# Kernel optimization log

Hardware: AMD Instinct MI355X
Metric: run time of the kernel (lower is better)

Reference implementation:

```python
import jax, jax.numpy as jnp
import numpy as np

BATCH = 128
IN_CH, OUT_CH = 64, 64
IN_DIM, OUT_DIM = 4096, 4096
IN_HALF = IN_DIM // 2 + 1    # 2049
OUT_HALF = OUT_DIM // 2 + 1  # 2049
MODES = max(IN_HALF, OUT_HALF)


def setup_inputs() -> dict:
    key = jax.random.key(0)
    k1, k2, k3 = jax.random.split(key, 3)
    scale = 1.0 / np.sqrt(IN_CH * OUT_CH)
    x = jax.random.normal(k1, (BATCH, IN_CH, IN_DIM), dtype=jnp.float32)
    # torch.rand(..., dtype=cfloat) draws U[0,1) for real and imag parts independently
    w_real = jax.random.uniform(k2, (IN_CH, OUT_CH, MODES), dtype=jnp.float32) * scale
    w_imag = jax.random.uniform(k3, (IN_CH, OUT_CH, MODES), dtype=jnp.float32) * scale
    b_real = jnp.zeros((OUT_CH, MODES), dtype=jnp.float32)
    b_imag = jnp.zeros((OUT_CH, MODES), dtype=jnp.float32)
    return {"x": x, "w_real": w_real, "w_imag": w_imag, "b_real": b_real, "b_imag": b_imag}


def _fftfreq_k(n):
    # torch.fft.fftfreq(n) * n -> integer wavenumbers [0,1,...,-1]
    return (jnp.fft.fftfreq(n) * n).astype(jnp.float32)


def reference(x, w_real, w_imag, b_real, b_imag):
    k_in = _fftfreq_k(IN_HALF)    # [IN_HALF]
    k_out = _fftfreq_k(OUT_HALF)  # [OUT_HALF]

    # --- shift_phase ---
    z = jnp.fft.rfft(x)                    # [B, Cin, IN_HALF] complex64
    phi = jnp.angle(z[..., 1])             # [B, Cin] phase of first nonzero mode
    z = z * jnp.exp(-1j * (phi[..., None] * k_in))  # align phases
    phi0 = phi[..., 0:1]                   # [B, 1]

    # pad mode axis up to MODES (no-op when IN_HALF == MODES)
    z = jnp.pad(z, ((0, 0), (0, 0), (0, MODES - IN_HALF)))

    # complex per-mode channel mixing + bias
    w = w_real + 1j * w_imag               # [Cin, Cout, MODES]
    b = b_real + 1j * b_imag               # [Cout, MODES]
    out_ft = jnp.einsum('bix,iox->box', z, w) + b
    out_ft = out_ft[..., :OUT_HALF]        # [B, Cout, OUT_HALF]

    # --- unshift_phase ---
    out_ft = out_ft * jnp.exp(1j * (phi0[..., None] * k_out))  # broadcast [B,1,OUT_HALF]
    return jnp.fft.irfft(out_ft, n=OUT_DIM)  # [B, Cout, OUT_DIM]
```

## Files before the change

kernel.cpp:

```cpp
#include <hip/hip_runtime.h>
#include <math.h>

#define NFFT 4096
#define MH   2048
#define HALF 2049
#define NSIG 8192
#define KT   32
#define NKT  65
#define PAD(e) ((e) + ((e) >> 3))

__device__ __forceinline__ float2 cmulf(float2 a, float2 b) {
  return make_float2(a.x*b.x - a.y*b.y, a.x*b.y + a.y*b.x);
}
__device__ __forceinline__ float2 f2add(float2 a, float2 b){ return make_float2(a.x+b.x, a.y+b.y); }
__device__ __forceinline__ float2 f2sub(float2 a, float2 b){ return make_float2(a.x-b.x, a.y-b.y); }
template<int S> __device__ __forceinline__ float2 mulJ(float2 v){
  return (S < 0) ? make_float2(v.y, -v.x) : make_float2(-v.y, v.x);
}
template<int S> __device__ __forceinline__ void dft4(const float2 a[4], float2 X[4]){
  float2 t0 = f2add(a[0],a[2]), t1 = f2sub(a[0],a[2]);
  float2 t2 = f2add(a[1],a[3]), t3 = f2sub(a[1],a[3]);
  X[0] = f2add(t0,t2); X[2] = f2sub(t0,t2);
  float2 j3 = mulJ<S>(t3);
  X[1] = f2add(t1,j3); X[3] = f2sub(t1,j3);
}
template<int S> __device__ __forceinline__ void dft8(const float2 x[8], float2 X[8]){
  float2 e[4] = {x[0],x[2],x[4],x[6]}, o[4] = {x[1],x[3],x[5],x[7]};
  float2 E[4], O[4]; dft4<S>(e,E); dft4<S>(o,O);
  const float c = 0.70710678118654752f;
  float2 o1 = cmulf(O[1], make_float2(c, (float)S*c));
  float2 o2 = mulJ<S>(O[2]);
  float2 o3 = cmulf(O[3], make_float2(-c, (float)S*c));
  X[0]=f2add(E[0],O[0]); X[4]=f2sub(E[0],O[0]);
  X[1]=f2add(E[1],o1);   X[5]=f2sub(E[1],o1);
  X[2]=f2add(E[2],o2);   X[6]=f2sub(E[2],o2);
  X[3]=f2add(E[3],o3);   X[7]=f2sub(E[3],o3);
}

template<int S>
__device__ __forceinline__ void fft2048(float2* buf, const int tid) {
  #pragma unroll
  for (int lg = 0; lg < 3; ++lg) {
    const int s  = 1 << (3*lg);
    const int q  = tid & (s - 1);
    const int ps = tid - q;
    float2 x[8];
    #pragma unroll
    for (int m = 0; m < 8; ++m) x[m] = buf[PAD(tid + (m << 8))];
    float2 X[8]; dft8<S>(x, X);
    const float th = (float)S * (6.283185307179586f / 2048.0f) * (float)ps;
    float sn, cs; __sincosf(th, &sn, &cs);
    const float2 w1 = make_float2(cs, sn);
    float2 wm = w1;
    X[1] = cmulf(X[1], w1);
    #pragma unroll
    for (int m = 2; m < 8; ++m) { wm = cmulf(wm, w1); X[m] = cmulf(X[m], wm); }
    __syncthreads();
    const int base = q + (ps << 3);
    #pragma unroll
    for (int t = 0; t < 8; ++t) buf[PAD(base + s*t)] = X[t];
    __syncthreads();
  }
  {
    float2 a0[4], a1[4], X0[4], X1[4];
    #pragma unroll
    for (int m = 0; m < 4; ++m) { a0[m] = buf[PAD(tid + (m<<9))]; a1[m] = buf[PAD(tid + 256 + (m<<9))]; }
    dft4<S>(a0, X0); dft4<S>(a1, X1);
    #pragma unroll
    for (int t = 0; t < 4; ++t) { buf[PAD(tid + (t<<9))] = X0[t]; buf[PAD(tid + 256 + (t<<9))] = X1[t]; }
    __syncthreads();
  }
}

__global__ __launch_bounds__(256) void k_rfft_phase(
    const float* __restrict__ x, float2* __restrict__ z, float* __restrict__ phi0) {
  __shared__ float2 buf[2304];
  const int bi  = blockIdx.x;
  const int tid = threadIdx.x;
  const float2* xp = (const float2*)(x + (size_t)bi * NFFT);
  for (int j = tid; j < MH; j += 256) buf[PAD(j)] = xp[j];
  __syncthreads();
  fft2048<-1>(buf, tid);

  {
    const float2 Y1 = buf[PAD(1)], Ym = buf[PAD(2047)];
    const float2 E = make_float2(0.5f*(Y1.x + Ym.x), 0.5f*(Y1.y - Ym.y));
    const float2 D = make_float2(0.5f*(Y1.x - Ym.x), 0.5f*(Y1.y + Ym.y));
    float sn, cs; __sincosf(6.283185307179586f / 4096.0f, &sn, &cs);
    const float2 Z1 = make_float2(E.x + (-sn*D.x + cs*D.y), E.y + (-sn*D.y - cs*D.x));
    const float phi = atan2f(Z1.y, Z1.x);
    if (tid == 0 && (bi & 63) == 0) phi0[bi >> 6] = phi;
    for (int k = tid; k < HALF; k += 256) {
      float2 Zk;
      if (k < MH) {
        const float2 Yk = buf[PAD(k)];
        const float2 Ymk = buf[PAD((MH - k) & (MH - 1))];
        const float2 Ek = make_float2(0.5f*(Yk.x + Ymk.x), 0.5f*(Yk.y - Ymk.y));
        const float2 Dk = make_float2(0.5f*(Yk.x - Ymk.x), 0.5f*(Yk.y + Ymk.y));
        float snk, csk; __sincosf(6.283185307179586f * (float)k / 4096.0f, &snk, &csk);
        Zk = make_float2(Ek.x + (-snk*Dk.x + csk*Dk.y), Ek.y + (-snk*Dk.y - csk*Dk.x));
      } else {
        const float2 Y0 = buf[PAD(0)];
        Zk = make_float2(Y0.x - Y0.y, 0.0f);
      }
      const int kin = (k <= 1024) ? k : k - HALF;
      double rev = (double)phi * (double)kin * 0.15915494309189535;
      rev -= rint(rev);
      const float thr = (float)(rev * 6.283185307179586);
      float snr, csr; __sincosf(thr, &snr, &csr);
      const float2 r = make_float2(Zk.x*csr + Zk.y*snr, Zk.y*csr - Zk.x*snr);
      z[((size_t)(k >> 5) * NSIG + bi) * KT + (k & 31)] = r;
    }
  }
}

__global__ __launch_bounds__(256) void k_gemm_mode(
    float2* __restrict__ zio,
    const float* __restrict__ wr, const float* __restrict__ wi,
    const float* __restrict__ br, const float* __restrict__ bim,
    const float* __restrict__ phi0) {
  __shared__ float4 zst[2][4][128];
  const int t  = threadIdx.x;
  const int kk = t & 31;
  const int g  = t >> 5;
  const int o0 = g * 8;
  const int kt = blockIdx.y;
  const int b0 = blockIdx.x * 4;
  const int k  = kt * KT + kk;
  const bool kvalid = (k < HALF);
  const int kc = kvalid ? k : (HALF - 1);

  const int sb = t >> 6;
  const int sh = t & 63;

  float2 acc[4][8];
  #pragma unroll
  for (int bb = 0; bb < 4; ++bb)
    #pragma unroll
    for (int oo = 0; oo < 8; ++oo) acc[bb][oo] = make_float2(0.f, 0.f);

  const size_t tilebase = (size_t)kt * NSIG * KT;

  {
    const float4* s4 = (const float4*)(zio + tilebase + (size_t)((b0 + sb) * 64) * KT);
    zst[0][sb][sh]      = s4[sh];
    zst[0][sb][sh + 64] = s4[sh + 64];
  }

  #pragma unroll 1
  for (int c = 0; c < 8; ++c) {
    float4 p0, p1;
    if (c < 7) {
      const float4* s4 = (const float4*)(zio + tilebase + (size_t)((b0 + sb) * 64 + (c + 1) * 8) * KT);
      p0 = s4[sh]; p1 = s4[sh + 64];
    }
    __syncthreads();
    #pragma unroll 2
    for (int il = 0; il < 8; ++il) {
      const int i = c * 8 + il;
      float2 zv[4];
      #pragma unroll
      for (int bb = 0; bb < 4; ++bb)
        zv[bb] = ((const float2*)&zst[c & 1][bb][0])[il * KT + kk];
      const float* wrp = wr + ((size_t)i * 64 + o0) * HALF + kc;
      const float* wip = wi + ((size_t)i * 64 + o0) * HALF + kc;
      float wvr[8], wvi[8];
      #pragma unroll
      for (int oo = 0; oo < 8; ++oo) { wvr[oo] = wrp[(size_t)oo * HALF]; wvi[oo] = wip[(size_t)oo * HALF]; }
      #pragma unroll
      for (int oo = 0; oo < 8; ++oo)
        #pragma unroll
        for (int bb = 0; bb < 4; ++bb) {
          acc[bb][oo].x += zv[bb].x * wvr[oo] - zv[bb].y * wvi[oo];
          acc[bb][oo].y += zv[bb].x * wvi[oo] + zv[bb].y * wvr[oo];
        }
    }
    if (c < 7) {
      zst[(c + 1) & 1][sb][sh]      = p0;
      zst[(c + 1) & 1][sb][sh + 64] = p1;
    }
  }
  __syncthreads();

  const int kout = (k <= 1024) ? k : k - HALF;
  #pragma unroll
  for (int bb = 0; bb < 4; ++bb) {
    double rev = (double)phi0[b0 + bb] * (double)kout * 0.15915494309189535;
    rev -= rint(rev);
    const float th = (float)(rev * 6.283185307179586);
    float sn, cs; __sincosf(th, &sn, &cs);
    const float2 rot = make_float2(cs, sn);
    #pragma unroll
    for (int oo = 0; oo < 8; ++oo) {
      const int o = o0 + oo;
      const float2 v = make_float2(acc[bb][oo].x + br[(size_t)o * HALF + kc],
                                   acc[bb][oo].y + bim[(size_t)o * HALF + kc]);
      if (kvalid)
        zio[tilebase + (size_t)((b0 + bb) * 64 + o) * KT + kk] = cmulf(v, rot);
    }
  }
}

__global__ __launch_bounds__(256) void k_irfft(
    const float2* __restrict__ oft, float* __restrict__ out) {
  __shared__ float2 buf[2304];
  const int bo  = blockIdx.x;
  const int tid = threadIdx.x;

  for (int k = tid; k <= 1024; k += 256) {
    const float2 Zk_raw = oft[((size_t)(k >> 5) * NSIG + bo) * KT + (k & 31)];
    if (k == 0) {
      const float2 Zn_raw = oft[((size_t)(MH >> 5) * NSIG + bo) * KT + 0];
      const float2 Zk = make_float2(Zk_raw.x, 0.f);
      const float2 Zm = make_float2(Zn_raw.x, 0.f);
      buf[PAD(0)] = make_float2(0.5f * (Zk.x + Zm.x), 0.5f * (Zk.x - Zm.x));
    } else {
      const int m = MH - k;
      const float2 Zm_raw = (k == 1024) ? Zk_raw
          : oft[((size_t)(m >> 5) * NSIG + bo) * KT + (m & 31)];
      {
        const float2 A = make_float2(Zk_raw.x + Zm_raw.x, Zk_raw.y - Zm_raw.y);
        const float2 D = make_float2(Zk_raw.x - Zm_raw.x, Zk_raw.y + Zm_raw.y);
        float sn, cs; __sincosf(6.283185307179586f * (float)k / 4096.0f, &sn, &cs);
        buf[PAD(k)] = make_float2(0.5f*(A.x + (-sn*D.x - cs*D.y)),
                                  0.5f*(A.y + (-sn*D.y + cs*D.x)));
      }
      if (k != 1024) {
        const float2 A = make_float2(Zm_raw.x + Zk_raw.x, Zm_raw.y - Zk_raw.y);
        const float2 D = make_float2(Zm_raw.x - Zk_raw.x, Zm_raw.y + Zk_raw.y);
        float sn, cs; __sincosf(6.283185307179586f * (float)m / 4096.0f, &sn, &cs);
        buf[PAD(m)] = make_float2(0.5f*(A.x + (-sn*D.x - cs*D.y)),
                                  0.5f*(A.y + (-sn*D.y + cs*D.x)));
      }
    }
  }
  __syncthreads();
  fft2048<1>(buf, tid);

  const float s = 1.0f / (float)MH;
  float2* op = (float2*)(out + (size_t)bo * NFFT);
  for (int n = tid; n < MH; n += 256) {
    const float2 y = buf[PAD(n)];
    op[n] = make_float2(y.x * s, y.y * s);
  }
}

extern "C" void kernel_launch(void* const* d_in, const int* in_sizes, int n_in,
                              void* d_out, int out_size, void* d_ws, size_t ws_size,
                              hipStream_t stream) {
  const float* x   = (const float*)d_in[0];
  const float* wr  = (const float*)d_in[1];
  const float* wi  = (const float*)d_in[2];
  const float* br  = (const float*)d_in[3];
  const float* bim = (const float*)d_in[4];
  float* out = (float*)d_out;

  char* ws = (char*)d_ws;
  float*  phi0 = (float*)ws;
  float2* zA   = (float2*)(ws + 4096);

  k_rfft_phase<<<NSIG, 256, 0, stream>>>(x, zA, phi0);
  k_gemm_mode<<<dim3(32, NKT), 256, 0, stream>>>(zA, wr, wi, br, bim, phi0);
  k_irfft<<<NSIG, 256, 0, stream>>>(zA, out);
}
```

Measured before the change: 630.2 us.

## Pack spectral weights into bf16 pairs in a transposed layout for mode GEMM

Result: slower. 1.005 ms (+59.4%).

```diff
diff --git a/kernel.cpp b/kernel.cpp
--- a/kernel.cpp
+++ b/kernel.cpp
@@ -70,6 +70,25 @@
     for (int t = 0; t < 4; ++t) { buf[PAD(tid + (t<<9))] = X0[t]; buf[PAD(tid + 256 + (t<<9))] = X1[t]; }
     __syncthreads();
   }
+}
+
+__device__ __forceinline__ unsigned short f2bf(float f){
+  unsigned int u = __float_as_uint(f);
+  u = (u + 0x7fffu + ((u >> 16) & 1u)) >> 16;
+  return (unsigned short)u;
+}
+
+__global__ __launch_bounds__(256) void k_wtrans(
+    const float* __restrict__ wr, const float* __restrict__ wi, unsigned int* __restrict__ wt) {
+  const int blk = blockIdx.x;
+  const int og = blk & 7, i = (blk >> 3) & 63, kt = blk >> 9;
+  const int t = threadIdx.x, kk = t & 31, oo = t >> 5;
+  const int o = og * 8 + oo;
+  const int k = kt * KT + kk;
+  const int kc = (k < HALF) ? k : (HALF - 1);
+  const size_t src = (size_t)(i * 64 + o) * HALF + kc;
+  const unsigned int u = (unsigned int)f2bf(wr[src]) | ((unsigned int)f2bf(wi[src]) << 16);
+  wt[(((size_t)kt * 64 + i) * 64 + o) * KT + kk] = u;
 }
 
 __global__ __launch_bounds__(256) void k_rfft_phase(
@@ -115,8 +134,7 @@
 }
 
 __global__ __launch_bounds__(256) void k_gemm_mode(
-    float2* __restrict__ zio,
-    const float* __restrict__ wr, const float* __restrict__ wi,
+    float2* __restrict__ zio, const unsigned int* __restrict__ wt,
     const float* __restrict__ br, const float* __restrict__ bim,
     const float* __restrict__ phi0) {
   __shared__ float4 zst[2][4][128];
@@ -140,6 +158,7 @@
     for (int oo = 0; oo < 8; ++oo) acc[bb][oo] = make_float2(0.f, 0.f);
 
   const size_t tilebase = (size_t)kt * NSIG * KT;
+  const unsigned int* wbase = wt + (((size_t)kt * 64) * 64 + o0) * KT + kk;
 
   {
     const float4* s4 = (const float4*)(zio + tilebase + (size_t)((b0 + sb) * 64) * KT);
@@ -162,18 +181,18 @@
       #pragma unroll
       for (int bb = 0; bb < 4; ++bb)
         zv[bb] = ((const float2*)&zst[c & 1][bb][0])[il * KT + kk];
-      const float* wrp = wr + ((size_t)i * 64 + o0) * HALF + kc;
-      const float* wip = wi + ((size_t)i * 64 + o0) * HALF + kc;
-      float wvr[8], wvi[8];
+      const unsigned int* wp = wbase + (size_t)i * 64 * KT;
       #pragma unroll
-      for (int oo = 0; oo < 8; ++oo) { wvr[oo] = wrp[(size_t)oo * HALF]; wvi[oo] = wip[(size_t)oo * HALF]; }
-      #pragma unroll
-      for (int oo = 0; oo < 8; ++oo)
+      for (int oo = 0; oo < 8; ++oo) {
+        const unsigned int wv = wp[oo * KT];
+        const float wrv = __uint_as_float(wv << 16);
+        const float wiv = __uint_as_float(wv & 0xffff0000u);
         #pragma unroll
         for (int bb = 0; bb < 4; ++bb) {
-          acc[bb][oo].x += zv[bb].x * wvr[oo] - zv[bb].y * wvi[oo];
-          acc[bb][oo].y += zv[bb].x * wvi[oo] + zv[bb].y * wvr[oo];
+          acc[bb][oo].x += zv[bb].x * wrv - zv[bb].y * wiv;
+          acc[bb][oo].y += zv[bb].x * wiv + zv[bb].y * wrv;
         }
+      }
     }
     if (c < 7) {
       zst[(c + 1) & 1][sb][sh]      = p0;
@@ -211,9 +230,7 @@
     const float2 Zk_raw = oft[((size_t)(k >> 5) * NSIG + bo) * KT + (k & 31)];
     if (k == 0) {
       const float2 Zn_raw = oft[((size_t)(MH >> 5) * NSIG + bo) * KT + 0];
-      const float2 Zk = make_float2(Zk_raw.x, 0.f);
-      const float2 Zm = make_float2(Zn_raw.x, 0.f);
-      buf[PAD(0)] = make_float2(0.5f * (Zk.x + Zm.x), 0.5f * (Zk.x - Zm.x));
+      buf[PAD(0)] = make_float2(0.5f * (Zk_raw.x + Zn_raw.x), 0.5f * (Zk_raw.x - Zn_raw.x));
     } else {
       const int m = MH - k;
       const float2 Zm_raw = (k == 1024) ? Zk_raw
@@ -256,10 +273,13 @@
   float* out = (float*)d_out;
 
   char* ws = (char*)d_ws;
-  float*  phi0 = (float*)ws;
-  float2* zA   = (float2*)(ws + 4096);
-
+  const size_t ZBYTES = (size_t)NKT * NSIG * KT * sizeof(float2);
+  float*        phi0 = (float*)ws;
+  float2*       zA   = (float2*)(ws + 4096);
+  unsigned int* wt   = (unsigned int*)(ws + 4096 + ZBYTES);
+
+  k_wtrans<<<NKT * 64 * 8, 256, 0, stream>>>(wr, wi, wt);
   k_rfft_phase<<<NSIG, 256, 0, stream>>>(x, zA, phi0);
-  k_gemm_mode<<<dim3(32, NKT), 256, 0, stream>>>(zA, wr, wi, br, bim, phi0);
+  k_gemm_mode<<<dim3(32, NKT), 256, 0, stream>>>(zA, wt, br, bim, phi0);
   k_irfft<<<NSIG, 256, 0, stream>>>(zA, out);
 }
```
